# Kernel optimization log

Measured on AMD Instinct MI355X. Metric: run time of the kernel, lower is better.

The kernel has to match this reference:

```python
import jax, jax.numpy as jnp
import numpy as np

NUM_HEADS = 16
EXP_DIM = 256
HIDDEN = 1024
B, S = 4, 2048


def setup_inputs() -> dict:
    key = jax.random.key(0)
    ks = jax.random.split(key, 16)
    sd = 0.02
    inp = {
        "x": jax.random.normal(ks[0], (B, S, HIDDEN), dtype=jnp.float32),
        "confidence": jax.random.uniform(ks[1], (B,), dtype=jnp.float32),
        "Wq": jax.random.normal(ks[2], (HIDDEN, HIDDEN), dtype=jnp.float32) * sd,
        "bq": jnp.zeros((HIDDEN,), dtype=jnp.float32),
        "Wk": jax.random.normal(ks[3], (HIDDEN, HIDDEN), dtype=jnp.float32) * sd,
        "bk": jnp.zeros((HIDDEN,), dtype=jnp.float32),
        "Wv": jax.random.normal(ks[4], (HIDDEN, HIDDEN), dtype=jnp.float32) * sd,
        "bv": jnp.zeros((HIDDEN,), dtype=jnp.float32),
        "Weq": jax.random.normal(ks[5], (HIDDEN, EXP_DIM), dtype=jnp.float32) * sd,
        "beq": jnp.zeros((EXP_DIM,), dtype=jnp.float32),
        "Wek": jax.random.normal(ks[6], (HIDDEN, EXP_DIM), dtype=jnp.float32) * sd,
        "bek": jnp.zeros((EXP_DIM,), dtype=jnp.float32),
        "Wo": jax.random.normal(ks[7], (HIDDEN, HIDDEN), dtype=jnp.float32) * sd,
        "bo": jnp.zeros((HIDDEN,), dtype=jnp.float32),
    }
    return inp


def reference(x, confidence, Wq, bq, Wk, bk, Wv, bv, Weq, beq, Wek, bek, Wo, bo):
    b, s, h = x.shape
    nh = NUM_HEADS
    hd = h // nh
    # Q/K/V projections -> [B, nh, S, hd]
    q = (x @ Wq + bq).reshape(b, s, nh, hd).transpose(0, 2, 1, 3)
    k = (x @ Wk + bk).reshape(b, s, nh, hd).transpose(0, 2, 1, 3)
    v = (x @ Wv + bv).reshape(b, s, nh, hd).transpose(0, 2, 1, 3)
    scores = jnp.einsum("bhqd,bhkd->bhqk", q, k) / jnp.sqrt(jnp.float32(hd))
    # Experience-based additive bias, confidence-weighted, shared across heads
    exp_q = x @ Weq + beq  # [B, S, E]
    exp_k = x @ Wek + bek  # [B, S, E]
    exp_scores = jnp.einsum("bqe,bke->bqk", exp_q, exp_k) / jnp.sqrt(jnp.float32(EXP_DIM))
    exp_scores = exp_scores * confidence[:, None, None]
    scores = scores + 0.3 * exp_scores[:, None, :, :]
    probs = jax.nn.softmax(scores, axis=-1)  # dropout in eval mode = identity
    ctx = jnp.einsum("bhqk,bhkd->bhqd", probs, v)
    ctx = ctx.transpose(0, 2, 1, 3).reshape(b, s, h)
    return ctx @ Wo + bo
```

## Files before the change

### kernel.cpp

```cpp
#include <hip/hip_runtime.h>

#define HIDDEN 1024
#define EXPD   256
#define NH     16
#define HD     64
#define BB     4
#define SS     2048
#define NTOK   (BB*SS)
#define NCAT   3584
#define QSCALE 0.18033688f

typedef __attribute__((ext_vector_type(8))) short short8;
typedef __attribute__((ext_vector_type(4))) float f32x4;
typedef __attribute__((ext_vector_type(4))) unsigned short us4;

__device__ __forceinline__ unsigned short f2b(float f) {
  unsigned int u = __float_as_uint(f);
  u += 0x7fffu + ((u >> 16) & 1u);
  return (unsigned short)(u >> 16);
}
__device__ __forceinline__ float b2f(unsigned short u) {
  return __uint_as_float(((unsigned int)u) << 16);
}
__device__ __forceinline__ f32x4 mfma_bf16(short8 a, short8 b, f32x4 c) {
  return __builtin_amdgcn_mfma_f32_16x16x32_bf16(a, b, c, 0, 0, 0);
}
__device__ __forceinline__ unsigned int cvt_pk(float lo, float hi) {
  unsigned int r;
  asm("v_cvt_pk_bf16_f32 %0, %1, %2" : "=v"(r) : "v"(lo), "v"(hi));
  return r;
}

__device__ __forceinline__ void gll16(const unsigned short* g, unsigned short* l) {
  __builtin_amdgcn_global_load_lds(
      (const __attribute__((address_space(1))) void*)g,
      (__attribute__((address_space(3))) void*)l, 16, 0, 0);
}

__device__ __forceinline__ short8 lds16(const unsigned short* base, int row, int bx) {
  return *reinterpret_cast<const short8*>(base + row * 64 + ((bx ^ (row & 7)) << 3));
}

__device__ __forceinline__ void stage64(const unsigned short* __restrict__ src,
                                        long long ldg, unsigned short* lds,
                                        int w, int lane) {
#pragma unroll
  for (int t = 0; t < 2; ++t) {
    const int rr = w * 16 + t * 8 + (lane >> 3);
    const int cc = ((lane & 7) ^ (rr & 7)) << 3;
    gll16(src + (long long)rr * ldg + cc, lds + (w * 16 + t * 8) * 64);
  }
}

__global__ __launch_bounds__(256) void prep_x(const float* __restrict__ x,
                                              unsigned short* __restrict__ A1) {
  const int idx4 = (blockIdx.x * 256 + threadIdx.x) * 4;
  const float4 xv = *reinterpret_cast<const float4*>(&x[idx4]);
  const int token = idx4 >> 10, c = idx4 & 1023;
  float vs[4] = {xv.x, xv.y, xv.z, xv.w};
  unsigned short hi[4], lo[4];
#pragma unroll
  for (int e = 0; e < 4; ++e) {
    unsigned short h = f2b(vs[e]);
    hi[e] = h;
    lo[e] = f2b(vs[e] - b2f(h));
  }
  uint2 hv, lv;
  hv.x = (unsigned int)hi[0] | ((unsigned int)hi[1] << 16);
  hv.y = (unsigned int)hi[2] | ((unsigned int)hi[3] << 16);
  lv.x = (unsigned int)lo[0] | ((unsigned int)lo[1] << 16);
  lv.y = (unsigned int)lo[2] | ((unsigned int)lo[3] << 16);
  *reinterpret_cast<uint2*>(&A1[token * 2048 + c]) = hv;
  *reinterpret_cast<uint2*>(&A1[token * 2048 + 1024 + c]) = lv;
}

__global__ void bias_cat(const float* __restrict__ bq, const float* __restrict__ bk,
                         const float* __restrict__ bv, const float* __restrict__ beq,
                         const float* __restrict__ bek, float* __restrict__ bcat) {
  const int n = blockIdx.x * 256 + threadIdx.x;
  if (n >= NCAT) return;
  float v;
  if (n < 1024) v = bq[n] * QSCALE;
  else if (n < 2048) v = bk[n - 1024];
  else if (n < 3072) v = bv[n - 2048];
  else if (n < 3328) v = beq[n - 3072];
  else v = bek[n - 3328];
  bcat[n] = v;
}

__global__ __launch_bounds__(256) void trans_w(const float* __restrict__ src, int C,
                                               unsigned short* __restrict__ dst, int dstld,
                                               int n_off, int dup, float wscale) {
  __shared__ unsigned short t[64 * 68];
  const int k0 = blockIdx.x * 64, c0 = blockIdx.y * 64;
  const int tid = threadIdx.x;
#pragma unroll
  for (int i = 0; i < 16; ++i) {
    int e = i * 256 + tid;
    int r = e >> 6, c = e & 63;
    t[r * 68 + c] = f2b(src[(k0 + r) * C + c0 + c] * wscale);
  }
  __syncthreads();
#pragma unroll
  for (int i = 0; i < 16; ++i) {
    int e = i * 256 + tid;
    int r2 = e >> 6, c2 = e & 63;
    unsigned short v = t[c2 * 68 + r2];
    dst[(n_off + c0 + r2) * dstld + k0 + c2] = v;
    if (dup) dst[(n_off + c0 + r2) * dstld + 1024 + k0 + c2] = v;
  }
}

__global__ __launch_bounds__(256) void trans_v(const unsigned short* __restrict__ QKVEE,
                                               unsigned short* __restrict__ Vt) {
  __shared__ unsigned short t[64 * 68];
  const int tok0 = blockIdx.x * 64, hc0 = blockIdx.y * 64;
  const int tid = threadIdx.x;
#pragma unroll
  for (int i = 0; i < 16; ++i) {
    int e = i * 256 + tid;
    int r = e >> 6, c = e & 63;
    t[r * 68 + c] = QKVEE[(long long)(tok0 + r) * NCAT + 2048 + hc0 + c];
  }
  __syncthreads();
#pragma unroll
  for (int i = 0; i < 16; ++i) {
    int e = i * 256 + tid;
    int r2 = e >> 6, c2 = e & 63;
    Vt[(long long)(hc0 + r2) * NTOK + tok0 + c2] = t[c2 * 68 + r2];
  }
}

template <int MODE>
__global__ __launch_bounds__(256) void gemm128(
    const unsigned short* __restrict__ A, long long sAz, int lda,
    const unsigned short* __restrict__ Bt, long long sBz, int ldb,
    void* __restrict__ Cv, long long sCz, int ldc,
    const float* __restrict__ bias, const float* __restrict__ cmul,
    float scale, int K) {
  __shared__ __align__(16) unsigned short As[128 * 64];
  __shared__ __align__(16) unsigned short Bs[128 * 64];
  const int tid = threadIdx.x;
  const int lane = tid & 63, w = tid >> 6;
  const int wm = (w >> 1) * 64, wn = (w & 1) * 64;
  int flat = blockIdx.y * gridDim.x + blockIdx.x;
  const int nwg = gridDim.x * gridDim.y;
  flat = (flat & 7) * (nwg >> 3) + (flat >> 3);
  const int m0 = (flat % gridDim.x) * 128, n0 = (flat / gridDim.x) * 128;
  const int z = blockIdx.z;
  A += (long long)z * sAz;
  Bt += (long long)z * sBz;

  f32x4 acc[4][4];
#pragma unroll
  for (int i = 0; i < 4; ++i)
#pragma unroll
    for (int j = 0; j < 4; ++j)
#pragma unroll
      for (int e = 0; e < 4; ++e) acc[i][j][e] = 0.0f;

  const int srow = lane >> 3;
  const int scol = (lane & 7) << 3;

  for (int k0 = 0; k0 < K; k0 += 64) {
#pragma unroll
    for (int t = 0; t < 4; ++t) {
      const int rr = w * 32 + t * 8 + srow;
      gll16(&A[(long long)(m0 + rr) * lda + k0 + scol], &As[(w * 32 + t * 8) * 64]);
      gll16(&Bt[(long long)(n0 + rr) * ldb + k0 + scol], &Bs[(w * 32 + t * 8) * 64]);
    }
    __syncthreads();
#pragma unroll
    for (int kk = 0; kk < 2; ++kk) {
      const int ko = kk * 32 + (lane >> 4) * 8;
      short8 af[4], bf[4];
#pragma unroll
      for (int mf = 0; mf < 4; ++mf)
        af[mf] = *reinterpret_cast<const short8*>(&As[(wm + mf * 16 + (lane & 15)) * 64 + ko]);
#pragma unroll
      for (int nf = 0; nf < 4; ++nf)
        bf[nf] = *reinterpret_cast<const short8*>(&Bs[(wn + nf * 16 + (lane & 15)) * 64 + ko]);
#pragma unroll
      for (int mf = 0; mf < 4; ++mf)
#pragma unroll
        for (int nf = 0; nf < 4; ++nf)
          acc[mf][nf] = mfma_bf16(af[mf], bf[nf], acc[mf][nf]);
    }
    __syncthreads();
  }

  const int rb = m0 + wm + ((lane >> 4) << 2);
  const int cb = n0 + wn + (lane & 15);
  float scl = scale;
  if (MODE == 1) scl *= cmul[z];
#pragma unroll
  for (int mf = 0; mf < 4; ++mf) {
#pragma unroll
    for (int nf = 0; nf < 4; ++nf) {
      const int col = cb + nf * 16;
      const int row0 = rb + mf * 16;
      if (MODE == 1) {
        unsigned short* C = (unsigned short*)Cv + (long long)z * sCz;
        us4 pk;
#pragma unroll
        for (int j = 0; j < 4; ++j) pk[j] = f2b(acc[mf][nf][j] * scl);
        *reinterpret_cast<us4*>(&C[(long long)col * ldc + row0]) = pk;
      } else if (MODE == 0) {
        unsigned short* C = (unsigned short*)Cv + (long long)z * sCz;
        const float bc = bias[col];
#pragma unroll
        for (int j = 0; j < 4; ++j)
          C[(long long)(row0 + j) * ldc + col] = f2b(acc[mf][nf][j] + bc);
      } else {
        float* C = (float*)Cv + (long long)z * sCz;
        const float bc = bias[col];
#pragma unroll
        for (int j = 0; j < 4; ++j)
          C[(long long)(row0 + j) * ldc + col] = acc[mf][nf][j] + bc;
      }
    }
  }
}

__global__ __launch_bounds__(256, 4) void attn_kernel(
    const unsigned short* __restrict__ QKVEE,
    const unsigned short* __restrict__ Vt,
    const unsigned short* __restrict__ expS,
    unsigned short* __restrict__ ctx) {
  __shared__ __align__(16) unsigned short Ks[64 * 64];
  __shared__ __align__(16) unsigned short Vs[64 * 64];
  __shared__ __align__(16) unsigned short Bs[64 * 64];

  const int tid = threadIdx.x, lane = tid & 63, w = tid >> 6;
  const int flat = blockIdx.x;
  const int pos = flat >> 3;
  const int h = pos & 15, b = (pos >> 4) & 3;
  const int qt = (flat & 7) + 8 * (pos >> 6);
  const int qbase = qt * 64;
  const long long tb = (long long)b * SS;

  const int c0 = lane & 15, g = lane >> 4, r0 = g * 4;
  const int qr = w * 16 + c0;

  short8 qf[2];
#pragma unroll
  for (int kk = 0; kk < 2; ++kk)
    qf[kk] = *reinterpret_cast<const short8*>(
        &QKVEE[(tb + qbase + qr) * NCAT + h * HD + kk * 32 + g * 8]);

  float m = -3.0e38f, l = 0.0f;
  f32x4 acc[4];
#pragma unroll
  for (int nf = 0; nf < 4; ++nf)
#pragma unroll
    for (int j = 0; j < 4; ++j) acc[nf][j] = 0.0f;

  for (int kb = 0; kb < SS; kb += 64) {
    stage64(QKVEE + (tb + kb) * NCAT + HIDDEN + h * HD, NCAT, Ks, w, lane);
    stage64(Vt + (long long)(h * HD) * NTOK + tb + kb, NTOK, Vs, w, lane);
    stage64(expS + (tb + qbase) * SS + kb, SS, Bs, w, lane);
    __syncthreads();

    f32x4 s[4];
#pragma unroll
    for (int nf = 0; nf < 4; ++nf)
#pragma unroll
      for (int j = 0; j < 4; ++j) s[nf][j] = 0.0f;
#pragma unroll
    for (int kk = 0; kk < 2; ++kk) {
      const int bx = kk * 4 + g;
#pragma unroll
      for (int nf = 0; nf < 4; ++nf) {
        short8 kf = lds16(Ks, nf * 16 + c0, bx);
        s[nf] = mfma_bf16(kf, qf[kk], s[nf]);
      }
    }

    float sv[4][4];
#pragma unroll
    for (int nf = 0; nf < 4; ++nf) {
      const int col = nf * 16 + r0;
      const us4 bb = *reinterpret_cast<const us4*>(
          &Bs[qr * 64 + (((col >> 3) ^ (qr & 7)) << 3) + (col & 7)]);
#pragma unroll
      for (int j = 0; j < 4; ++j) sv[nf][j] = s[nf][j] + b2f(bb[j]);
    }

    float t0 = fmaxf(fmaxf(sv[0][0], sv[0][1]), fmaxf(sv[0][2], sv[0][3]));
    float t1 = fmaxf(fmaxf(sv[1][0], sv[1][1]), fmaxf(sv[1][2], sv[1][3]));
    float t2 = fmaxf(fmaxf(sv[2][0], sv[2][1]), fmaxf(sv[2][2], sv[2][3]));
    float t3 = fmaxf(fmaxf(sv[3][0], sv[3][1]), fmaxf(sv[3][2], sv[3][3]));
    float rmax = fmaxf(fmaxf(t0, t1), fmaxf(t2, t3));
    rmax = fmaxf(rmax, __shfl_xor(rmax, 16));
    rmax = fmaxf(rmax, __shfl_xor(rmax, 32));

    if (__any(rmax > m + 8.0f)) {
      const float mn = fmaxf(m, rmax);
      const float sc = __builtin_amdgcn_exp2f(m - mn);
      m = mn;
      l *= sc;
      float scj[4];
#pragma unroll
      for (int j = 0; j < 4; ++j) scj[j] = __shfl(sc, r0 + j);
#pragma unroll
      for (int nf = 0; nf < 4; ++nf)
#pragma unroll
        for (int j = 0; j < 4; ++j) acc[nf][j] *= scj[j];
    }

    unsigned int wds[4][2];
    float ps0 = 0.f, ps1 = 0.f;
#pragma unroll
    for (int nf = 0; nf < 4; ++nf) {
      const float p0 = __builtin_amdgcn_exp2f(sv[nf][0] - m);
      const float p1 = __builtin_amdgcn_exp2f(sv[nf][1] - m);
      const float p2 = __builtin_amdgcn_exp2f(sv[nf][2] - m);
      const float p3 = __builtin_amdgcn_exp2f(sv[nf][3] - m);
      wds[nf][0] = cvt_pk(p0, p1);
      wds[nf][1] = cvt_pk(p2, p3);
      ps0 += p0 + p1;
      ps1 += p2 + p3;
    }
    float psum = ps0 + ps1;
    psum += __shfl_xor(psum, 16);
    psum += __shfl_xor(psum, 32);
    l += psum;

#pragma unroll
    for (int kk = 0; kk < 2; ++kk) {
      union { unsigned int u[4]; short8 v8; } pa;
      pa.u[0] = wds[2 * kk][0];
      pa.u[1] = wds[2 * kk][1];
      pa.u[2] = wds[2 * kk + 1][0];
      pa.u[3] = wds[2 * kk + 1][1];
#pragma unroll
      for (int nf = 0; nf < 4; ++nf) {
        const int rowd = nf * 16 + c0;
        const int cA = kk * 32 + r0;
        const int cB = cA + 16;
        union { us4 h2[2]; short8 v8; } vf;
        vf.h2[0] = *reinterpret_cast<const us4*>(
            &Vs[rowd * 64 + (((cA >> 3) ^ (rowd & 7)) << 3) + (cA & 7)]);
        vf.h2[1] = *reinterpret_cast<const us4*>(
            &Vs[rowd * 64 + (((cB >> 3) ^ (rowd & 7)) << 3) + (cB & 7)]);
        acc[nf] = mfma_bf16(pa.v8, vf.v8, acc[nf]);
      }
    }
    __syncthreads();
  }

  float linv[4];
#pragma unroll
  for (int j = 0; j < 4; ++j) linv[j] = 1.0f / __shfl(l, r0 + j);
#pragma unroll
  for (int nf = 0; nf < 4; ++nf)
#pragma unroll
    for (int j = 0; j < 4; ++j) {
      const int qrow = qbase + w * 16 + r0 + j;
      const int d = nf * 16 + c0;
      ctx[(tb + qrow) * HIDDEN + h * HD + d] = f2b(acc[nf][j] * linv[j]);
    }
}

extern "C" void kernel_launch(void* const* d_in, const int* in_sizes, int n_in,
                              void* d_out, int out_size, void* d_ws, size_t ws_size,
                              hipStream_t stream) {
  const float* x    = (const float*)d_in[0];
  const float* conf = (const float*)d_in[1];
  const float* Wq   = (const float*)d_in[2];
  const float* bq   = (const float*)d_in[3];
  const float* Wk   = (const float*)d_in[4];
  const float* bk   = (const float*)d_in[5];
  const float* Wv   = (const float*)d_in[6];
  const float* bv   = (const float*)d_in[7];
  const float* Weq  = (const float*)d_in[8];
  const float* beq  = (const float*)d_in[9];
  const float* Wek  = (const float*)d_in[10];
  const float* bek  = (const float*)d_in[11];
  const float* Wo   = (const float*)d_in[12];
  const float* bo   = (const float*)d_in[13];

  char* ws = (char*)d_ws;
  unsigned short* A1    = (unsigned short*)(ws);
  unsigned short* WcatT = (unsigned short*)(ws + 33554432);
  float*          bcat  = (float*)(ws + 48234496);
  unsigned short* WoT   = (unsigned short*)(ws + 48250880);
  unsigned short* QKVEE = (unsigned short*)(ws + 50348032);
  unsigned short* Vt    = (unsigned short*)(ws + 109068288);
  unsigned short* ctx   = (unsigned short*)(ws + 125845504);
  unsigned short* expS  = (unsigned short*)d_out;

  prep_x<<<dim3(8192), dim3(256), 0, stream>>>(x, A1);
  bias_cat<<<dim3(14), dim3(256), 0, stream>>>(bq, bk, bv, beq, bek, bcat);
  trans_w<<<dim3(16, 16), dim3(256), 0, stream>>>(Wq, 1024, WcatT, 2048, 0, 1, QSCALE);
  trans_w<<<dim3(16, 16), dim3(256), 0, stream>>>(Wk, 1024, WcatT, 2048, 1024, 1, 1.0f);
  trans_w<<<dim3(16, 16), dim3(256), 0, stream>>>(Wv, 1024, WcatT, 2048, 2048, 1, 1.0f);
  trans_w<<<dim3(16, 4),  dim3(256), 0, stream>>>(Weq, 256, WcatT, 2048, 3072, 1, 1.0f);
  trans_w<<<dim3(16, 4),  dim3(256), 0, stream>>>(Wek, 256, WcatT, 2048, 3328, 1, 1.0f);
  trans_w<<<dim3(16, 16), dim3(256), 0, stream>>>(Wo, 1024, WoT, 1024, 0, 0, 1.0f);

  gemm128<0><<<dim3(64, 28), dim3(256), 0, stream>>>(
      A1, 0, 2048, WcatT, 0, 2048, QKVEE, 0, NCAT, bcat, nullptr, 1.0f, 2048);

  trans_v<<<dim3(128, 16), dim3(256), 0, stream>>>(QKVEE, Vt);

  gemm128<1><<<dim3(16, 16, 4), dim3(256), 0, stream>>>(
      QKVEE + 3328, (long long)SS * NCAT, NCAT,
      QKVEE + 3072, (long long)SS * NCAT, NCAT,
      expS, (long long)SS * SS, SS, nullptr, conf,
      0.3f * 1.44269504f / 16.0f, 256);

  attn_kernel<<<dim3(2048), dim3(256), 0, stream>>>(QKVEE, Vt, expS, ctx);

  gemm128<2><<<dim3(64, 8), dim3(256), 0, stream>>>(
      ctx, 0, 1024, WoT, 0, 1024, d_out, 0, 1024, bo, nullptr, 1.0f, 1024);
}
```

Measured before the change: 535.8 us.

## Add triple-buffered 256x128 GEMM kernel for QKV and output projections

Introduces a new 512-thread GEMM with 256x128 tiles and a three-stage LDS ring. Global-to-LDS async loads for the next stage are interleaved with MFMA work, using setprio and a single barrier per k-step. The QKV projection and output projection now use this kernel instead of the 128x128 double-buffered one. Larger tiles improve operand reuse and the deeper pipeline hides load latency, at the cost of more LDS per block (144KB for two blocks) and lower occupancy.

```diff
diff --git a/kernel.cpp b/kernel.cpp
--- a/kernel.cpp
+++ b/kernel.cpp
@@ -50,6 +50,13 @@
     const int cc = ((lane & 7) ^ (rr & 7)) << 3;
     gll16(src + (long long)rr * ldg + cc, lds + (w * 16 + t * 8) * 64);
   }
+}
+
+__device__ __forceinline__ void g2l_call(const unsigned short* __restrict__ g,
+                                         long long ldg, unsigned short* lds, int tid) {
+  const int r = tid >> 3;
+  const int c = ((tid & 7) ^ (r & 7)) << 3;
+  gll16(g + (long long)r * ldg + c, lds + (tid >> 6) * 512);
 }
 
 __global__ __launch_bounds__(256) void prep_x(const float* __restrict__ x,
@@ -128,6 +135,122 @@
     int e = i * 256 + tid;
     int r2 = e >> 6, c2 = e & 63;
     Vt[(long long)(hc0 + r2) * NTOK + tok0 + c2] = t[c2 * 68 + r2];
+  }
+}
+
+template <int MODE>
+__global__ __launch_bounds__(512, 2) void gemm256(
+    const unsigned short* __restrict__ A, int lda,
+    const unsigned short* __restrict__ Bt, int ldb,
+    void* __restrict__ Cv, int ldc,
+    const float* __restrict__ bias, int K, int nbn) {
+  __shared__ __align__(16) unsigned short As[3 * 256 * 64];
+  __shared__ __align__(16) unsigned short Bs[3 * 128 * 64];
+  const int tid = threadIdx.x, lane = tid & 63, w8 = tid >> 6;
+  int flat = blockIdx.x;
+  const int nwg = gridDim.x;
+  flat = (flat & 7) * (nwg >> 3) + (flat >> 3);
+  const int m0 = (flat / nbn) * 256, n0 = (flat % nbn) * 128;
+  const int NT = K >> 6;
+
+  const int R0 = (w8 & 3) * 64, C0 = (w8 >> 2) * 64;
+  const int fr = lane & 15, fg = lane >> 4;
+
+  f32x4 acc[4][4];
+#pragma unroll
+  for (int i = 0; i < 4; ++i)
+#pragma unroll
+    for (int j = 0; j < 4; ++j)
+#pragma unroll
+      for (int e = 0; e < 4; ++e) acc[i][j][e] = 0.0f;
+
+#pragma unroll
+  for (int p = 0; p < 2; ++p) {
+#pragma unroll
+    for (int c = 0; c < 4; ++c)
+      g2l_call(A + (long long)(m0 + c * 64) * lda + p * 64, lda,
+               As + p * 16384 + c * 4096, tid);
+#pragma unroll
+    for (int c = 0; c < 2; ++c)
+      g2l_call(Bt + (long long)(n0 + c * 64) * ldb + p * 64, ldb,
+               Bs + p * 8192 + c * 4096, tid);
+  }
+  asm volatile("s_waitcnt vmcnt(6)" ::: "memory");
+  __builtin_amdgcn_s_barrier();
+  __builtin_amdgcn_sched_barrier(0);
+
+  int tc = 0, td = 2, ts = 2;
+  for (int t = 0; t < NT; ++t) {
+    const unsigned short* Ab = As + tc * 16384;
+    const unsigned short* Bb = Bs + tc * 8192;
+    const int ks0 = ts * 64;
+    unsigned short* Ad = As + td * 16384;
+    unsigned short* Bd = Bs + td * 8192;
+
+    {
+      short8 af[4], bf[4];
+#pragma unroll
+      for (int mf = 0; mf < 4; ++mf) af[mf] = lds16(Ab, R0 + mf * 16 + fr, fg);
+#pragma unroll
+      for (int nf = 0; nf < 4; ++nf) bf[nf] = lds16(Bb, C0 + nf * 16 + fr, fg);
+#pragma unroll
+      for (int c = 0; c < 3; ++c)
+        g2l_call(A + (long long)(m0 + c * 64) * lda + ks0, lda, Ad + c * 4096, tid);
+      __builtin_amdgcn_s_setprio(1);
+#pragma unroll
+      for (int mf = 0; mf < 4; ++mf)
+#pragma unroll
+        for (int nf = 0; nf < 4; ++nf)
+          acc[mf][nf] = mfma_bf16(af[mf], bf[nf], acc[mf][nf]);
+      __builtin_amdgcn_s_setprio(0);
+    }
+    {
+      short8 af[4], bf[4];
+#pragma unroll
+      for (int mf = 0; mf < 4; ++mf) af[mf] = lds16(Ab, R0 + mf * 16 + fr, 4 + fg);
+#pragma unroll
+      for (int nf = 0; nf < 4; ++nf) bf[nf] = lds16(Bb, C0 + nf * 16 + fr, 4 + fg);
+      g2l_call(A + (long long)(m0 + 192) * lda + ks0, lda, Ad + 12288, tid);
+#pragma unroll
+      for (int c = 0; c < 2; ++c)
+        g2l_call(Bt + (long long)(n0 + c * 64) * ldb + ks0, ldb, Bd + c * 4096, tid);
+      __builtin_amdgcn_s_setprio(1);
+#pragma unroll
+      for (int mf = 0; mf < 4; ++mf)
+#pragma unroll
+        for (int nf = 0; nf < 4; ++nf)
+          acc[mf][nf] = mfma_bf16(af[mf], bf[nf], acc[mf][nf]);
+      __builtin_amdgcn_s_setprio(0);
+    }
+    asm volatile("s_waitcnt vmcnt(6)" ::: "memory");
+    __builtin_amdgcn_s_barrier();
+    __builtin_amdgcn_sched_barrier(0);
+    tc = (tc == 2) ? 0 : tc + 1;
+    td = (td == 2) ? 0 : td + 1;
+    ts = (ts + 1 == NT) ? 0 : ts + 1;
+  }
+
+  const int rb = m0 + R0 + fg * 4;
+  const int cb = n0 + C0 + fr;
+#pragma unroll
+  for (int mf = 0; mf < 4; ++mf) {
+#pragma unroll
+    for (int nf = 0; nf < 4; ++nf) {
+      const int col = cb + nf * 16;
+      const int row0 = rb + mf * 16;
+      const float bc = bias[col];
+      if (MODE == 0) {
+        unsigned short* C = (unsigned short*)Cv;
+#pragma unroll
+        for (int j = 0; j < 4; ++j)
+          C[(long long)(row0 + j) * ldc + col] = f2b(acc[mf][nf][j] + bc);
+      } else {
+        float* C = (float*)Cv;
+#pragma unroll
+        for (int j = 0; j < 4; ++j)
+          C[(long long)(row0 + j) * ldc + col] = acc[mf][nf][j] + bc;
+      }
+    }
   }
 }
 
@@ -205,18 +328,6 @@
 #pragma unroll
         for (int j = 0; j < 4; ++j) pk[j] = f2b(acc[mf][nf][j] * scl);
         *reinterpret_cast<us4*>(&C[(long long)col * ldc + row0]) = pk;
-      } else if (MODE == 0) {
-        unsigned short* C = (unsigned short*)Cv + (long long)z * sCz;
-        const float bc = bias[col];
-#pragma unroll
-        for (int j = 0; j < 4; ++j)
-          C[(long long)(row0 + j) * ldc + col] = f2b(acc[mf][nf][j] + bc);
-      } else {
-        float* C = (float*)Cv + (long long)z * sCz;
-        const float bc = bias[col];
-#pragma unroll
-        for (int j = 0; j < 4; ++j)
-          C[(long long)(row0 + j) * ldc + col] = acc[mf][nf][j] + bc;
       }
     }
   }
@@ -399,8 +510,8 @@
   trans_w<<<dim3(16, 4),  dim3(256), 0, stream>>>(Wek, 256, WcatT, 2048, 3328, 1, 1.0f);
   trans_w<<<dim3(16, 16), dim3(256), 0, stream>>>(Wo, 1024, WoT, 1024, 0, 0, 1.0f);
 
-  gemm128<0><<<dim3(64, 28), dim3(256), 0, stream>>>(
-      A1, 0, 2048, WcatT, 0, 2048, QKVEE, 0, NCAT, bcat, nullptr, 1.0f, 2048);
+  gemm256<0><<<dim3(896), dim3(512), 0, stream>>>(
+      A1, 2048, WcatT, 2048, QKVEE, NCAT, bcat, 2048, 28);
 
   trans_v<<<dim3(128, 16), dim3(256), 0, stream>>>(QKVEE, Vt);
 
@@ -412,6 +523,6 @@
 
   attn_kernel<<<dim3(2048), dim3(256), 0, stream>>>(QKVEE, Vt, expS, ctx);
 
-  gemm128<2><<<dim3(64, 8), dim3(256), 0, stream>>>(
-      ctx, 0, 1024, WoT, 0, 1024, d_out, 0, 1024, bo, nullptr, 1.0f, 1024);
-}
+  gemm256<2><<<dim3(256), dim3(512), 0, stream>>>(
+      ctx, 1024, WoT, 1024, d_out, 1024, bo, 1024, 8);
+}
```

Result: faster. 476.4 us (-11.1%).
